# Optimization experiments

Measured on AMD Instinct MI355X. Metric: run time of the kernel, lower is better.

Reference implementation:

```python
import jax, jax.numpy as jnp
import numpy as np

N_USER = 100000
N_ITEM = 100000
SUPP = 10000
B = 1024
L = 50
S = 256
H = 4
E = 64
HID = 64


def setup_inputs() -> dict:
    key = jax.random.key(0)
    ks = jax.random.split(key, 32)
    f32 = jnp.float32
    inp = {}
    # forward int args
    inp["x"] = jax.random.randint(ks[0], (B, 2), 0, N_USER)
    inp["src_his"] = jax.random.randint(ks[1], (B, L), 0, N_ITEM)
    inp["src_hl"] = jax.random.randint(ks[2], (B,), 0, L)
    inp["tgt_his"] = jax.random.randint(ks[3], (B, L), 0, N_ITEM)
    inp["tgt_hl"] = jax.random.randint(ks[4], (B,), 0, L)
    # precomputed neighbor sampling: [2 get_user_emb calls, H heads, B, S]
    inp["sample_idx"] = jax.random.randint(ks[5], (2, H, B, S), 0, SUPP)
    inp["supp_users"] = jax.random.randint(ks[6], (SUPP,), 0, N_USER)
    # embedding tables (xavier-ish small scale)
    inp["src_user_emb"] = jax.random.normal(ks[7], (N_USER, E), f32) * 0.1
    inp["src_item_emb"] = jax.random.normal(ks[8], (N_ITEM, E), f32) * 0.1
    inp["tgt_user_emb"] = jax.random.normal(ks[9], (N_USER, E), f32) * 0.1
    inp["tgt_item_emb"] = jax.random.normal(ks[10], (N_ITEM, E), f32) * 0.1
    # attention / aggregation weights, stored [in, out]
    s = 1.0 / np.sqrt(E)
    inp["W_att_w"] = jax.random.normal(ks[11], (E, E), f32) * s
    inp["W_att_b"] = jnp.full((E,), 0.1, f32)
    inp["W_agg_w"] = jax.random.normal(ks[12], (E, E), f32) * s
    # per-head GAT projections, batched over heads
    inp["Wq"] = jax.random.normal(ks[13], (H, E, E), f32) * s
    inp["Wk"] = jax.random.normal(ks[14], (H, E, E), f32) * s
    inp["Wv"] = jax.random.normal(ks[15], (H, E, E), f32) * s
    inp["W_out"] = jax.random.normal(ks[16], (H * E, E), f32) * (1.0 / np.sqrt(H * E))
    # scoring MLP
    inp["l1_w"] = jax.random.normal(ks[17], (2 * E, HID), f32) * (1.0 / np.sqrt(2 * E))
    inp["l1_b"] = jnp.full((HID,), 0.1, f32)
    inp["l2_w"] = jax.random.normal(ks[18], (HID, E), f32) * (1.0 / np.sqrt(HID))
    inp["l2_b"] = jnp.full((E,), 0.1, f32)
    inp["l3_w"] = jax.random.normal(ks[19], (E, 1), f32) * s
    inp["l3_b"] = jnp.full((1,), 0.1, f32)
    return inp


def reference(x, src_his, src_hl, tgt_his, tgt_hl, sample_idx, supp_users,
              src_user_emb, src_item_emb, tgt_user_emb, tgt_item_emb,
              W_att_w, W_att_b, W_agg_w, Wq, Wk, Wv, W_out,
              l1_w, l1_b, l2_w, l2_b, l3_w, l3_b):
    user_id = x[:, 0]
    item_id = x[:, 1]

    def user_fea_encode(his, hl, user_table):
        # NOTE: original always gathers from src_model.item_embedding (even for tgt)
        Lh = his.shape[1]
        valid = jnp.arange(Lh)[None, :] < hl[:, None]          # [B,L]
        hist = src_item_emb[his] * valid[..., None]             # [B,L,E], padded rows zeroed
        u = user_table[user_id]                                 # [B,E]
        keyt = jnp.tanh(hist @ W_att_w + W_att_b)               # [B,L,E]
        pad = hist.sum(-1) == 0                                 # [B,L]
        att = jnp.einsum('ble,be->bl', keyt, u)
        # faithful masked_softmax: masked scores set to 0 BEFORE exp (exp(0)=1 still contributes)
        att = jnp.where(pad, 0.0, att)
        e = jnp.exp(att)
        att = e / (jnp.sum(e, axis=1, keepdims=True) + 1e-12)
        out = jnp.einsum('bl,ble->be', att, hist)
        return out @ W_agg_w                                    # W_agg has no bias

    def get_user_emb(fea, idx):
        # idx: [H,B,S] indices into supp_users; all heads batched in one einsum chain
        neigh = tgt_user_emb[supp_users[idx]]                   # [H,B,S,E]
        q = jnp.einsum('be,heo->hbo', fea, Wq)                  # [H,B,O]
        k = jnp.einsum('hbse,heo->hbso', neigh, Wk)             # [H,B,S,O]
        attn = jax.nn.softmax(jnp.einsum('hbo,hbso->hbs', q, k), axis=-1)
        ctx = jnp.einsum('hbs,hbso->hbo', attn, k)              # weighted sum over neighbors
        g = jnp.einsum('hbo,hop->hbp', ctx, Wv)                 # [H,B,O]
        g = jnp.transpose(g, (1, 0, 2)).reshape(fea.shape[0], -1)  # concat heads -> [B,H*O]
        return g @ W_out

    user_src_fea = user_fea_encode(src_his, src_hl, src_user_emb)
    user_emb = get_user_emb(user_src_fea, sample_idx[0])
    item_emb = tgt_item_emb[item_id]
    user_tgt_fea = user_fea_encode(tgt_his, tgt_hl, tgt_user_emb)
    hybrid_tgt_emb = get_user_emb(user_tgt_fea, sample_idx[1])

    x_t = jnp.concatenate([hybrid_tgt_emb, item_emb], axis=1)
    x1_t = jnp.tanh(x_t @ l1_w + l1_b)
    x2_t = jnp.tanh(x1_t @ l2_w + l2_b)
    x3_t = (x2_t @ l3_w + l3_b).reshape(-1)

    output = jnp.sum(user_emb * item_emb, axis=1)
    out_emb_s = user_emb * item_emb
    # (output, output_t, out_emb_s, out_emb_t); train=False branch (sim/domain heads are None)
    return (output, x3_t, out_emb_s, x2_t)
```

## Files before the change

kernel.cpp:

```cpp
#include <hip/hip_runtime.h>

constexpr int B    = 1024;
constexpr int L    = 50;
constexpr int S    = 256;
constexpr int H    = 4;
constexpr int E    = 64;
constexpr int HID  = 64;
constexpr int SUPP = 10000;

__device__ __forceinline__ float tanh_fast(float x) {
    const float xc = fminf(fmaxf(x, -15.0f), 15.0f);
    const float e  = __expf(2.0f * xc);
    return (e - 1.0f) * __builtin_amdgcn_rcpf(e + 1.0f);
}

__device__ __forceinline__ float lanebc(float v, int l) {
    return __int_as_float(__builtin_amdgcn_readlane(__float_as_int(v), l));
}

__global__ __launch_bounds__(256) void pre_kernel(
    const int* __restrict__ x,
    const int* __restrict__ src_his,
    const int* __restrict__ src_hl,
    const int* __restrict__ tgt_his,
    const int* __restrict__ tgt_hl,
    const float* __restrict__ item_emb,
    const float* __restrict__ src_user_emb,
    const float* __restrict__ tgt_user_emb,
    const int* __restrict__ supp_users,
    const float* __restrict__ W_att_w,
    const float* __restrict__ W_att_b,
    const float* __restrict__ W_agg_w,
    const float* __restrict__ Wq,
    const float* __restrict__ Wk,
    float* __restrict__ qout,
    float* __restrict__ K_supp)
{
    const int tid  = threadIdx.x;
    const int lane = tid & 63;
    const int wave = tid >> 6;

    if (blockIdx.y == 2) {
        __shared__ __align__(16) float sEvw[4][E];
        const int h = wave;
        float wcol[E];
#pragma unroll
        for (int i = 0; i < E; i++) wcol[i] = Wk[h * E * E + i * E + lane];

        int j = blockIdx.x;
        float ev = tgt_user_emb[(size_t)supp_users[j] * E + lane];
#pragma unroll 1
        while (j < SUPP) {
            const int jn = j + (int)gridDim.x;
            float evn = 0.0f;
            if (jn < SUPP)
                evn = tgt_user_emb[(size_t)supp_users[jn] * E + lane];
            sEvw[wave][lane] = ev;
            const float4* e4 = (const float4*)&sEvw[wave][0];
            float a0 = 0.f, a1 = 0.f, a2 = 0.f, a3 = 0.f;
#pragma unroll
            for (int k = 0; k < 16; k++) {
                const float4 v = e4[k];
                a0 = fmaf(v.x, wcol[4 * k + 0], a0);
                a1 = fmaf(v.y, wcol[4 * k + 1], a1);
                a2 = fmaf(v.z, wcol[4 * k + 2], a2);
                a3 = fmaf(v.w, wcol[4 * k + 3], a3);
            }
            K_supp[((size_t)h * SUPP + j) * E + lane] = (a0 + a1) + (a2 + a3);
            j = jn;
            ev = evn;
        }
        return;
    }

    __shared__ __align__(16) float sHist[L * E];
    __shared__ float sAtt[64];
    __shared__ float sPart[4][E];
    __shared__ float sOut[E];

    const int b    = blockIdx.x;
    const int call = blockIdx.y;

    const int* his = call ? tgt_his : src_his;
    const int* hl  = call ? tgt_hl  : src_hl;
    const float* user_table = call ? tgt_user_emb : src_user_emb;

    float wcol[E];
#pragma unroll
    for (int i = 0; i < E; i++) wcol[i] = W_att_w[i * E + lane];

    const int uid    = x[2 * b];
    const float uv   = user_table[(size_t)uid * E + lane];
    const float bias = W_att_b[lane];
    const int hlen   = hl[b];

#pragma unroll 1
    for (int l = wave; l < L; l += 4)
        if (l >= hlen && lane == 0) sAtt[l] = 0.0f;

    if (wave < hlen) {
        int l = wave;
        float hv = item_emb[(size_t)his[b * L + l] * E + lane];
#pragma unroll 1
        while (true) {
            const int ln = l + 4;
            float hvn = 0.0f;
            if (ln < hlen)
                hvn = item_emb[(size_t)his[b * L + ln] * E + lane];
            sHist[l * E + lane] = hv;
            const float4* hrow = (const float4*)&sHist[l * E];
            float a0 = bias, a1 = 0.f, a2 = 0.f, a3 = 0.f;
#pragma unroll
            for (int k = 0; k < 16; k++) {
                const float4 h4 = hrow[k];
                a0 = fmaf(h4.x, wcol[4 * k + 0], a0);
                a1 = fmaf(h4.y, wcol[4 * k + 1], a1);
                a2 = fmaf(h4.z, wcol[4 * k + 2], a2);
                a3 = fmaf(h4.w, wcol[4 * k + 3], a3);
            }
            float part = tanh_fast((a0 + a1) + (a2 + a3)) * uv;
#pragma unroll
            for (int off = 32; off; off >>= 1) part += __shfl_xor(part, off);
            if (lane == 0) sAtt[l] = part;
            l = ln;
            if (l >= hlen) break;
            hv = hvn;
        }
    }
    __syncthreads();

    const float vex = (lane < L) ? __expf(sAtt[lane]) : 0.0f;
    float sden = vex;
#pragma unroll
    for (int off = 32; off; off >>= 1) sden += __shfl_xor(sden, off);
    const float rden = __builtin_amdgcn_rcpf(sden + 1e-12f);

    float c = 0.0f;
#pragma unroll 1
    for (int l = wave; l < hlen; l += 4)
        c = fmaf(lanebc(vex, l) * rden, sHist[l * E + lane], c);
    sPart[wave][lane] = c;
    __syncthreads();
    if (tid < E) sOut[tid] = sPart[0][tid] + sPart[1][tid] + sPart[2][tid] + sPart[3][tid];
    __syncthreads();

    float g = 0.0f;
#pragma unroll
    for (int k = 0; k < 16; k++) {
        const int i = wave * 16 + k;
        g += sOut[i] * W_agg_w[i * E + lane];
    }
    sPart[wave][lane] = g;
    __syncthreads();

    const float fval = sPart[0][lane] + sPart[1][lane] + sPart[2][lane] + sPart[3][lane];
    const float* Wqh = Wq + wave * E * E;
    float q0 = 0.f, q1 = 0.f, q2 = 0.f, q3 = 0.f;
#pragma unroll
    for (int i = 0; i < E; i += 4) {
        q0 = fmaf(lanebc(fval, i + 0), Wqh[(i + 0) * E + lane], q0);
        q1 = fmaf(lanebc(fval, i + 1), Wqh[(i + 1) * E + lane], q1);
        q2 = fmaf(lanebc(fval, i + 2), Wqh[(i + 2) * E + lane], q2);
        q3 = fmaf(lanebc(fval, i + 3), Wqh[(i + 3) * E + lane], q3);
    }
    qout[(((call * H) + wave) * B + b) * E + lane] = (q0 + q1) + (q2 + q3);
}

__global__ __launch_bounds__(256) void attn_kernel(
    const int* __restrict__ sample_idx,
    const float* __restrict__ K_supp,
    const float* __restrict__ qarr,
    const float* __restrict__ Wv,
    float* __restrict__ gout)
{
    __shared__ float sRed[8];
    __shared__ float sCtx[4][E];
    __shared__ float sC[E];
    __shared__ float sG[4][E];

    const int n    = blockIdx.x;
    const int xcd  = n & 7;
    const int h    = xcd >> 1;
    const int call = xcd & 1;
    const int b    = n >> 3;
    const int tid  = threadIdx.x;
    const int lane = tid & 63;
    const int wave = tid >> 6;
    const int u    = lane & 15;
    const int rsub = lane >> 4;
    const int s0   = wave * 64;

    const int* idx = sample_idx + (((call * H) + h) * B + b) * S;
    const float* Kh = K_supp + (size_t)h * SUPP * E;
    const float4 qu = *(const float4*)(qarr + ((size_t)(((call * H) + h) * B + b)) * E + 4 * u);

    int jr[16];
#pragma unroll
    for (int i = 0; i < 16; i++) jr[i] = idx[s0 + 4 * i + rsub];
    float4 kreg[16];
#pragma unroll
    for (int i = 0; i < 16; i++)
        kreg[i] = *(const float4*)(Kh + (size_t)jr[i] * E + 4 * u);

    float mylogit = 0.0f;
#pragma unroll
    for (int i = 0; i < 16; i++) {
        float part = kreg[i].x * qu.x + kreg[i].y * qu.y
                   + kreg[i].z * qu.z + kreg[i].w * qu.w;
#pragma unroll
        for (int off = 1; off < 16; off <<= 1) part += __shfl_xor(part, off);
        mylogit = (u == i) ? part : mylogit;
    }

    float m = mylogit;
#pragma unroll
    for (int off = 32; off; off >>= 1) m = fmaxf(m, __shfl_xor(m, off));
    if (lane == 0) sRed[wave] = m;
    __syncthreads();
    const float mx = fmaxf(fmaxf(sRed[0], sRed[1]), fmaxf(sRed[2], sRed[3]));
    const float ex = __expf(mylogit - mx);
    float sm = ex;
#pragma unroll
    for (int off = 32; off; off >>= 1) sm += __shfl_xor(sm, off);
    if (lane == 0) sRed[4 + wave] = sm;
    __syncthreads();
    const float denom = sRed[4] + sRed[5] + sRed[6] + sRed[7];
    const float pval = ex / denom;

    float4 cacc = make_float4(0.0f, 0.0f, 0.0f, 0.0f);
#pragma unroll
    for (int i = 0; i < 16; i++) {
        const float p = __shfl(pval, (lane & 48) + i);
        cacc.x += p * kreg[i].x;
        cacc.y += p * kreg[i].y;
        cacc.z += p * kreg[i].z;
        cacc.w += p * kreg[i].w;
    }
#pragma unroll
    for (int off = 16; off <= 32; off <<= 1) {
        cacc.x += __shfl_xor(cacc.x, off);
        cacc.y += __shfl_xor(cacc.y, off);
        cacc.z += __shfl_xor(cacc.z, off);
        cacc.w += __shfl_xor(cacc.w, off);
    }
    if (lane < 16) *(float4*)(&sCtx[wave][u * 4]) = cacc;
    __syncthreads();
    if (wave == 0) {
        sC[lane] = sCtx[0][lane] + sCtx[1][lane] + sCtx[2][lane] + sCtx[3][lane];
    }
    __syncthreads();

    const float* Wvh = Wv + h * E * E;
    float g = 0.0f;
#pragma unroll
    for (int k = 0; k < 16; k++) {
        const int c = wave * 16 + k;
        g += sC[c] * Wvh[c * E + lane];
    }
    sG[wave][lane] = g;
    __syncthreads();
    if (wave == 0) {
        gout[((size_t)(call * B) + b) * (H * E) + h * E + lane] =
            sG[0][lane] + sG[1][lane] + sG[2][lane] + sG[3][lane];
    }
}

__global__ __launch_bounds__(256) void final_kernel(
    const int* __restrict__ x,
    const float* __restrict__ tgt_item_emb,
    const float* __restrict__ gsrc,
    const float* __restrict__ gtgt,
    const float* __restrict__ W_out,
    const float* __restrict__ l1_w,
    const float* __restrict__ l1_b,
    const float* __restrict__ l2_w,
    const float* __restrict__ l2_b,
    const float* __restrict__ l3_w,
    const float* __restrict__ l3_b,
    float* __restrict__ out)
{
    __shared__ float sPart[4][E];
    __shared__ float sHyb[E];
    __shared__ float sItem[E];
    __shared__ float sX1[HID];

    const int b    = blockIdx.x;
    const int tid  = threadIdx.x;
    const int lane = tid & 63;
    const int wave = tid >> 6;

    if (tid < E) {
        const int item = x[2 * b + 1];
        sItem[tid] = tgt_item_emb[(size_t)item * E + tid];
    }

    const float* grow = (wave < 2) ? (gsrc + (size_t)b * (H * E))
                                   : (gtgt + (size_t)b * (H * E));
    const int i0 = (wave & 1) * 128;
    {
        const float4* g4 = (const float4*)(grow + i0);
        float a0 = 0.0f, a1 = 0.0f, a2 = 0.0f, a3 = 0.0f;
#pragma unroll
        for (int k = 0; k < 32; k++) {
            const float4 v = g4[k];
            const float* wr = W_out + (i0 + 4 * k) * E + lane;
            a0 += v.x * wr[0];
            a1 += v.y * wr[E];
            a2 += v.z * wr[2 * E];
            a3 += v.w * wr[3 * E];
        }
        sPart[wave][lane] = (a0 + a1) + (a2 + a3);
    }
    __syncthreads();

    if (wave == 0) {
        const float ue = sPart[0][lane] + sPart[1][lane];
        const float prod = ue * sItem[lane];
        out[2 * B + b * E + lane] = prod;
        float s = prod;
#pragma unroll
        for (int off = 32; off; off >>= 1) s += __shfl_xor(s, off);
        if (lane == 0) out[b] = s;
    }
    if (wave == 1) {
        sHyb[lane] = sPart[2][lane] + sPart[3][lane];
    }
    __syncthreads();

    float a1 = 0.0f;
#pragma unroll
    for (int k = 0; k < 32; k++) {
        const int i = wave * 32 + k;
        const float v = (i < 64) ? sHyb[i] : sItem[i - 64];
        a1 += v * l1_w[i * HID + lane];
    }
    sPart[wave][lane] = a1;
    __syncthreads();

    if (wave == 0) {
        const float a = l1_b[lane] + sPart[0][lane] + sPart[1][lane]
                      + sPart[2][lane] + sPart[3][lane];
        sX1[lane] = tanh_fast(a);
    }
    __syncthreads();

    if (wave == 0) {
        float a = l2_b[lane];
#pragma unroll
        for (int i = 0; i < HID; i++) a += sX1[i] * l2_w[i * E + lane];
        const float x2 = tanh_fast(a);
        out[2 * B + B * E + b * E + lane] = x2;
        float p = x2 * l3_w[lane];
#pragma unroll
        for (int off = 32; off; off >>= 1) p += __shfl_xor(p, off);
        if (lane == 0) out[B + b] = p + l3_b[0];
    }
}

extern "C" void kernel_launch(void* const* d_in, const int* in_sizes, int n_in,
                              void* d_out, int out_size, void* d_ws, size_t ws_size,
                              hipStream_t stream) {
    const int*   x            = (const int*)d_in[0];
    const int*   src_his      = (const int*)d_in[1];
    const int*   src_hl       = (const int*)d_in[2];
    const int*   tgt_his      = (const int*)d_in[3];
    const int*   tgt_hl       = (const int*)d_in[4];
    const int*   sample_idx   = (const int*)d_in[5];
    const int*   supp_users   = (const int*)d_in[6];
    const float* src_user_emb = (const float*)d_in[7];
    const float* src_item_emb = (const float*)d_in[8];
    const float* tgt_user_emb = (const float*)d_in[9];
    const float* tgt_item_emb = (const float*)d_in[10];
    const float* W_att_w      = (const float*)d_in[11];
    const float* W_att_b      = (const float*)d_in[12];
    const float* W_agg_w      = (const float*)d_in[13];
    const float* Wq           = (const float*)d_in[14];
    const float* Wk           = (const float*)d_in[15];
    const float* Wv           = (const float*)d_in[16];
    const float* W_out        = (const float*)d_in[17];
    const float* l1_w         = (const float*)d_in[18];
    const float* l1_b         = (const float*)d_in[19];
    const float* l2_w         = (const float*)d_in[20];
    const float* l2_b         = (const float*)d_in[21];
    const float* l3_w         = (const float*)d_in[22];
    const float* l3_b         = (const float*)d_in[23];

    float* ws      = (float*)d_ws;
    float* qarr    = ws;
    float* K_supp  = qarr + 2 * H * B * E;
    float* garr    = K_supp + H * SUPP * E;
    float* out     = (float*)d_out;

    pre_kernel<<<dim3(B, 3), 256, 0, stream>>>(
        x, src_his, src_hl, tgt_his, tgt_hl, src_item_emb,
        src_user_emb, tgt_user_emb, supp_users,
        W_att_w, W_att_b, W_agg_w, Wq, Wk, qarr, K_supp);
    attn_kernel<<<dim3(B * H * 2), 256, 0, stream>>>(
        sample_idx, K_supp, qarr, Wv, garr);
    final_kernel<<<dim3(B), 256, 0, stream>>>(
        x, tgt_item_emb, garr, garr + B * H * E, W_out,
        l1_w, l1_b, l2_w, l2_b, l3_w, l3_b, out);
}
```

Baseline: 254.8 us.

## Fuse attention and final MLP kernels with single-wave online softmax per head

Merges the attention kernel and the final scoring kernel into one 512-thread block per batch row. Each wave now handles one (call, head) pair and walks its 256 neighbors in four chunks with an online softmax, so no cross-wave reductions are needed. The per-head outputs stay in shared memory instead of round-tripping through a global workspace, and one launch is removed. In exchange, each block loops over its neighbors serially with fewer blocks overall (1024 vs 8192), which reduces memory-level parallelism for the gather of K rows.

```diff
diff --git a/kernel.cpp b/kernel.cpp
--- a/kernel.cpp
+++ b/kernel.cpp
@@ -166,110 +166,13 @@
     qout[(((call * H) + wave) * B + b) * E + lane] = (q0 + q1) + (q2 + q3);
 }
 
-__global__ __launch_bounds__(256) void attn_kernel(
+__global__ __launch_bounds__(512) void attn_final_kernel(
     const int* __restrict__ sample_idx,
     const float* __restrict__ K_supp,
     const float* __restrict__ qarr,
     const float* __restrict__ Wv,
-    float* __restrict__ gout)
-{
-    __shared__ float sRed[8];
-    __shared__ float sCtx[4][E];
-    __shared__ float sC[E];
-    __shared__ float sG[4][E];
-
-    const int n    = blockIdx.x;
-    const int xcd  = n & 7;
-    const int h    = xcd >> 1;
-    const int call = xcd & 1;
-    const int b    = n >> 3;
-    const int tid  = threadIdx.x;
-    const int lane = tid & 63;
-    const int wave = tid >> 6;
-    const int u    = lane & 15;
-    const int rsub = lane >> 4;
-    const int s0   = wave * 64;
-
-    const int* idx = sample_idx + (((call * H) + h) * B + b) * S;
-    const float* Kh = K_supp + (size_t)h * SUPP * E;
-    const float4 qu = *(const float4*)(qarr + ((size_t)(((call * H) + h) * B + b)) * E + 4 * u);
-
-    int jr[16];
-#pragma unroll
-    for (int i = 0; i < 16; i++) jr[i] = idx[s0 + 4 * i + rsub];
-    float4 kreg[16];
-#pragma unroll
-    for (int i = 0; i < 16; i++)
-        kreg[i] = *(const float4*)(Kh + (size_t)jr[i] * E + 4 * u);
-
-    float mylogit = 0.0f;
-#pragma unroll
-    for (int i = 0; i < 16; i++) {
-        float part = kreg[i].x * qu.x + kreg[i].y * qu.y
-                   + kreg[i].z * qu.z + kreg[i].w * qu.w;
-#pragma unroll
-        for (int off = 1; off < 16; off <<= 1) part += __shfl_xor(part, off);
-        mylogit = (u == i) ? part : mylogit;
-    }
-
-    float m = mylogit;
-#pragma unroll
-    for (int off = 32; off; off >>= 1) m = fmaxf(m, __shfl_xor(m, off));
-    if (lane == 0) sRed[wave] = m;
-    __syncthreads();
-    const float mx = fmaxf(fmaxf(sRed[0], sRed[1]), fmaxf(sRed[2], sRed[3]));
-    const float ex = __expf(mylogit - mx);
-    float sm = ex;
-#pragma unroll
-    for (int off = 32; off; off >>= 1) sm += __shfl_xor(sm, off);
-    if (lane == 0) sRed[4 + wave] = sm;
-    __syncthreads();
-    const float denom = sRed[4] + sRed[5] + sRed[6] + sRed[7];
-    const float pval = ex / denom;
-
-    float4 cacc = make_float4(0.0f, 0.0f, 0.0f, 0.0f);
-#pragma unroll
-    for (int i = 0; i < 16; i++) {
-        const float p = __shfl(pval, (lane & 48) + i);
-        cacc.x += p * kreg[i].x;
-        cacc.y += p * kreg[i].y;
-        cacc.z += p * kreg[i].z;
-        cacc.w += p * kreg[i].w;
-    }
-#pragma unroll
-    for (int off = 16; off <= 32; off <<= 1) {
-        cacc.x += __shfl_xor(cacc.x, off);
-        cacc.y += __shfl_xor(cacc.y, off);
-        cacc.z += __shfl_xor(cacc.z, off);
-        cacc.w += __shfl_xor(cacc.w, off);
-    }
-    if (lane < 16) *(float4*)(&sCtx[wave][u * 4]) = cacc;
-    __syncthreads();
-    if (wave == 0) {
-        sC[lane] = sCtx[0][lane] + sCtx[1][lane] + sCtx[2][lane] + sCtx[3][lane];
-    }
-    __syncthreads();
-
-    const float* Wvh = Wv + h * E * E;
-    float g = 0.0f;
-#pragma unroll
-    for (int k = 0; k < 16; k++) {
-        const int c = wave * 16 + k;
-        g += sC[c] * Wvh[c * E + lane];
-    }
-    sG[wave][lane] = g;
-    __syncthreads();
-    if (wave == 0) {
-        gout[((size_t)(call * B) + b) * (H * E) + h * E + lane] =
-            sG[0][lane] + sG[1][lane] + sG[2][lane] + sG[3][lane];
-    }
-}
-
-__global__ __launch_bounds__(256) void final_kernel(
     const int* __restrict__ x,
     const float* __restrict__ tgt_item_emb,
-    const float* __restrict__ gsrc,
-    const float* __restrict__ gtgt,
     const float* __restrict__ W_out,
     const float* __restrict__ l1_w,
     const float* __restrict__ l1_b,
@@ -279,42 +182,123 @@
     const float* __restrict__ l3_b,
     float* __restrict__ out)
 {
-    __shared__ float sPart[4][E];
+    __shared__ __align__(16) float sCtxW[8][E];
+    __shared__ __align__(16) float sG[2][H * E];
+    __shared__ float sPart[8][E];
+    __shared__ float sItem[E];
     __shared__ float sHyb[E];
-    __shared__ float sItem[E];
     __shared__ float sX1[HID];
 
     const int b    = blockIdx.x;
     const int tid  = threadIdx.x;
     const int lane = tid & 63;
     const int wave = tid >> 6;
-
-    if (tid < E) {
-        const int item = x[2 * b + 1];
-        sItem[tid] = tgt_item_emb[(size_t)item * E + tid];
-    }
-
-    const float* grow = (wave < 2) ? (gsrc + (size_t)b * (H * E))
-                                   : (gtgt + (size_t)b * (H * E));
-    const int i0 = (wave & 1) * 128;
+    const int call = wave >> 2;
+    const int h    = wave & 3;
+    const int u    = lane & 15;
+    const int rsub = lane >> 4;
+
+    if (tid < E) sItem[tid] = tgt_item_emb[(size_t)x[2 * b + 1] * E + tid];
+
+    const int* idx = sample_idx + (((call * H) + h) * B + b) * S;
+    const float* Kh = K_supp + (size_t)h * SUPP * E;
+    const float4 qu = *(const float4*)(qarr + ((size_t)(((call * H) + h) * B + b)) * E + 4 * u);
+
+    float m = -1e30f, d = 0.0f;
+    float4 cacc = make_float4(0.0f, 0.0f, 0.0f, 0.0f);
+#pragma unroll 1
+    for (int c = 0; c < 4; c++) {
+        int jr[16];
+#pragma unroll
+        for (int i = 0; i < 16; i++) jr[i] = idx[64 * c + 4 * i + rsub];
+        float4 kreg[16];
+#pragma unroll
+        for (int i = 0; i < 16; i++)
+            kreg[i] = *(const float4*)(Kh + (size_t)jr[i] * E + 4 * u);
+
+        float lg = 0.0f;
+#pragma unroll
+        for (int i = 0; i < 16; i++) {
+            float part = kreg[i].x * qu.x + kreg[i].y * qu.y
+                       + kreg[i].z * qu.z + kreg[i].w * qu.w;
+#pragma unroll
+            for (int off = 1; off < 16; off <<= 1) part += __shfl_xor(part, off);
+            lg = (u == i) ? part : lg;
+        }
+
+        float cm = lg;
+#pragma unroll
+        for (int off = 32; off; off >>= 1) cm = fmaxf(cm, __shfl_xor(cm, off));
+        const float mn    = fmaxf(m, cm);
+        const float scale = __expf(m - mn);
+        const float ex    = __expf(lg - mn);
+        float cs = ex;
+#pragma unroll
+        for (int off = 32; off; off >>= 1) cs += __shfl_xor(cs, off);
+        d = d * scale + cs;
+        cacc.x *= scale; cacc.y *= scale; cacc.z *= scale; cacc.w *= scale;
+#pragma unroll
+        for (int i = 0; i < 16; i++) {
+            const float p = __shfl(ex, (lane & 48) + i);
+            cacc.x = fmaf(p, kreg[i].x, cacc.x);
+            cacc.y = fmaf(p, kreg[i].y, cacc.y);
+            cacc.z = fmaf(p, kreg[i].z, cacc.z);
+            cacc.w = fmaf(p, kreg[i].w, cacc.w);
+        }
+        m = mn;
+    }
+#pragma unroll
+    for (int off = 16; off <= 32; off <<= 1) {
+        cacc.x += __shfl_xor(cacc.x, off);
+        cacc.y += __shfl_xor(cacc.y, off);
+        cacc.z += __shfl_xor(cacc.z, off);
+        cacc.w += __shfl_xor(cacc.w, off);
+    }
+    const float rd = 1.0f / d;
+    if (rsub == 0) {
+        float4 cv;
+        cv.x = cacc.x * rd; cv.y = cacc.y * rd;
+        cv.z = cacc.z * rd; cv.w = cacc.w * rd;
+        *(float4*)(&sCtxW[wave][u * 4]) = cv;
+    }
     {
-        const float4* g4 = (const float4*)(grow + i0);
-        float a0 = 0.0f, a1 = 0.0f, a2 = 0.0f, a3 = 0.0f;
-#pragma unroll
-        for (int k = 0; k < 32; k++) {
+        const float4* cw = (const float4*)&sCtxW[wave][0];
+        const float* Wvh = Wv + h * E * E;
+        float g0 = 0.f, g1 = 0.f, g2 = 0.f, g3 = 0.f;
+#pragma unroll
+        for (int k = 0; k < 16; k++) {
+            const float4 cv = cw[k];
+            const float* wr = Wvh + (4 * k) * E + lane;
+            g0 = fmaf(cv.x, wr[0],     g0);
+            g1 = fmaf(cv.y, wr[E],     g1);
+            g2 = fmaf(cv.z, wr[2 * E], g2);
+            g3 = fmaf(cv.w, wr[3 * E], g3);
+        }
+        sG[call][h * E + lane] = (g0 + g1) + (g2 + g3);
+    }
+    __syncthreads();
+
+    {
+        const int p = wave >> 2;
+        const int q = wave & 3;
+        const float4* g4 = (const float4*)&sG[p][q * 64];
+        float a0 = 0.f, a1 = 0.f, a2 = 0.f, a3 = 0.f;
+#pragma unroll
+        for (int k = 0; k < 16; k++) {
             const float4 v = g4[k];
-            const float* wr = W_out + (i0 + 4 * k) * E + lane;
-            a0 += v.x * wr[0];
-            a1 += v.y * wr[E];
-            a2 += v.z * wr[2 * E];
-            a3 += v.w * wr[3 * E];
+            const float* wr = W_out + (q * 64 + 4 * k) * E + lane;
+            a0 = fmaf(v.x, wr[0],     a0);
+            a1 = fmaf(v.y, wr[E],     a1);
+            a2 = fmaf(v.z, wr[2 * E], a2);
+            a3 = fmaf(v.w, wr[3 * E], a3);
         }
         sPart[wave][lane] = (a0 + a1) + (a2 + a3);
     }
     __syncthreads();
 
     if (wave == 0) {
-        const float ue = sPart[0][lane] + sPart[1][lane];
+        const float ue = (sPart[0][lane] + sPart[1][lane])
+                       + (sPart[2][lane] + sPart[3][lane]);
         const float prod = ue * sItem[lane];
         out[2 * B + b * E + lane] = prod;
         float s = prod;
@@ -323,23 +307,27 @@
         if (lane == 0) out[b] = s;
     }
     if (wave == 1) {
-        sHyb[lane] = sPart[2][lane] + sPart[3][lane];
-    }
-    __syncthreads();
-
-    float a1 = 0.0f;
-#pragma unroll
-    for (int k = 0; k < 32; k++) {
-        const int i = wave * 32 + k;
-        const float v = (i < 64) ? sHyb[i] : sItem[i - 64];
-        a1 += v * l1_w[i * HID + lane];
-    }
-    sPart[wave][lane] = a1;
+        sHyb[lane] = (sPart[4][lane] + sPart[5][lane])
+                   + (sPart[6][lane] + sPart[7][lane]);
+    }
+    __syncthreads();
+
+    {
+        float a1v = 0.0f;
+#pragma unroll
+        for (int k = 0; k < 16; k++) {
+            const int i = wave * 16 + k;
+            const float v = (i < 64) ? sHyb[i] : sItem[i - 64];
+            a1v = fmaf(v, l1_w[i * HID + lane], a1v);
+        }
+        sPart[wave][lane] = a1v;
+    }
     __syncthreads();
 
     if (wave == 0) {
-        const float a = l1_b[lane] + sPart[0][lane] + sPart[1][lane]
-                      + sPart[2][lane] + sPart[3][lane];
+        float a = l1_b[lane];
+#pragma unroll
+        for (int w = 0; w < 8; w++) a += sPart[w][lane];
         sX1[lane] = tanh_fast(a);
     }
     __syncthreads();
@@ -347,7 +335,7 @@
     if (wave == 0) {
         float a = l2_b[lane];
 #pragma unroll
-        for (int i = 0; i < HID; i++) a += sX1[i] * l2_w[i * E + lane];
+        for (int i = 0; i < HID; i++) a = fmaf(sX1[i], l2_w[i * E + lane], a);
         const float x2 = tanh_fast(a);
         out[2 * B + B * E + b * E + lane] = x2;
         float p = x2 * l3_w[lane];
@@ -388,16 +376,13 @@
     float* ws      = (float*)d_ws;
     float* qarr    = ws;
     float* K_supp  = qarr + 2 * H * B * E;
-    float* garr    = K_supp + H * SUPP * E;
     float* out     = (float*)d_out;
 
     pre_kernel<<<dim3(B, 3), 256, 0, stream>>>(
         x, src_his, src_hl, tgt_his, tgt_hl, src_item_emb,
         src_user_emb, tgt_user_emb, supp_users,
         W_att_w, W_att_b, W_agg_w, Wq, Wk, qarr, K_supp);
-    attn_kernel<<<dim3(B * H * 2), 256, 0, stream>>>(
-        sample_idx, K_supp, qarr, Wv, garr);
-    final_kernel<<<dim3(B), 256, 0, stream>>>(
-        x, tgt_item_emb, garr, garr + B * H * E, W_out,
+    attn_final_kernel<<<dim3(B), 512, 0, stream>>>(
+        sample_idx, K_supp, qarr, Wv, x, tgt_item_emb, W_out,
         l1_w, l1_b, l2_w, l2_b, l3_w, l3_b, out);
 }
```

Measured after the change: 287.4 us. 12.8% more time.

## Widen pre_kernel to 512 threads, splitting history, aggregation and Q projection across 8 waves

Applied to the files above, without the earlier changes.

The pre-processing kernel moves from 4 to 8 waves per block. History rows are strided by 8 and the W_agg reduction is split 8 ways. The Q projection splits each head's input dimension across two waves and adds their partial sums through shared memory. The K_supp branch handles two support users per block iteration. The aim is more parallelism and latency hiding per block, at the cost of extra barriers and per-thread register pressure (wcol[64]) under the 512-thread launch bound, which could lower occupancy.

```diff
diff --git a/kernel.cpp b/kernel.cpp
--- a/kernel.cpp
+++ b/kernel.cpp
@@ -18,7 +18,7 @@
     return __int_as_float(__builtin_amdgcn_readlane(__float_as_int(v), l));
 }
 
-__global__ __launch_bounds__(256) void pre_kernel(
+__global__ __launch_bounds__(512) void pre_kernel(
     const int* __restrict__ x,
     const int* __restrict__ src_his,
     const int* __restrict__ src_hl,
@@ -41,17 +41,18 @@
     const int wave = tid >> 6;
 
     if (blockIdx.y == 2) {
-        __shared__ __align__(16) float sEvw[4][E];
-        const int h = wave;
+        __shared__ __align__(16) float sEvw[8][E];
+        const int h = wave & 3;
         float wcol[E];
 #pragma unroll
         for (int i = 0; i < E; i++) wcol[i] = Wk[h * E * E + i * E + lane];
 
-        int j = blockIdx.x;
-        float ev = tgt_user_emb[(size_t)supp_users[j] * E + lane];
+        int j = 2 * blockIdx.x + (wave >> 2);
+        const int jstride = 2 * (int)gridDim.x;
+        float ev = (j < SUPP) ? tgt_user_emb[(size_t)supp_users[j] * E + lane] : 0.0f;
 #pragma unroll 1
         while (j < SUPP) {
-            const int jn = j + (int)gridDim.x;
+            const int jn = j + jstride;
             float evn = 0.0f;
             if (jn < SUPP)
                 evn = tgt_user_emb[(size_t)supp_users[jn] * E + lane];
@@ -75,7 +76,7 @@
 
     __shared__ __align__(16) float sHist[L * E];
     __shared__ float sAtt[64];
-    __shared__ float sPart[4][E];
+    __shared__ float sPart[8][E];
     __shared__ float sOut[E];
 
     const int b    = blockIdx.x;
@@ -95,7 +96,7 @@
     const int hlen   = hl[b];
 
 #pragma unroll 1
-    for (int l = wave; l < L; l += 4)
+    for (int l = wave; l < L; l += 8)
         if (l >= hlen && lane == 0) sAtt[l] = 0.0f;
 
     if (wave < hlen) {
@@ -103,7 +104,7 @@
         float hv = item_emb[(size_t)his[b * L + l] * E + lane];
 #pragma unroll 1
         while (true) {
-            const int ln = l + 4;
+            const int ln = l + 8;
             float hvn = 0.0f;
             if (ln < hlen)
                 hvn = item_emb[(size_t)his[b * L + ln] * E + lane];
@@ -137,33 +138,55 @@
 
     float c = 0.0f;
 #pragma unroll 1
-    for (int l = wave; l < hlen; l += 4)
+    for (int l = wave; l < hlen; l += 8)
         c = fmaf(lanebc(vex, l) * rden, sHist[l * E + lane], c);
     sPart[wave][lane] = c;
     __syncthreads();
-    if (tid < E) sOut[tid] = sPart[0][tid] + sPart[1][tid] + sPart[2][tid] + sPart[3][tid];
-    __syncthreads();
-
-    float g = 0.0f;
-#pragma unroll
-    for (int k = 0; k < 16; k++) {
-        const int i = wave * 16 + k;
-        g += sOut[i] * W_agg_w[i * E + lane];
-    }
-    sPart[wave][lane] = g;
-    __syncthreads();
-
-    const float fval = sPart[0][lane] + sPart[1][lane] + sPart[2][lane] + sPart[3][lane];
-    const float* Wqh = Wq + wave * E * E;
-    float q0 = 0.f, q1 = 0.f, q2 = 0.f, q3 = 0.f;
-#pragma unroll
-    for (int i = 0; i < E; i += 4) {
-        q0 = fmaf(lanebc(fval, i + 0), Wqh[(i + 0) * E + lane], q0);
-        q1 = fmaf(lanebc(fval, i + 1), Wqh[(i + 1) * E + lane], q1);
-        q2 = fmaf(lanebc(fval, i + 2), Wqh[(i + 2) * E + lane], q2);
-        q3 = fmaf(lanebc(fval, i + 3), Wqh[(i + 3) * E + lane], q3);
-    }
-    qout[(((call * H) + wave) * B + b) * E + lane] = (q0 + q1) + (q2 + q3);
+    if (tid < E) {
+        sOut[tid] = ((sPart[0][tid] + sPart[1][tid]) + (sPart[2][tid] + sPart[3][tid]))
+                  + ((sPart[4][tid] + sPart[5][tid]) + (sPart[6][tid] + sPart[7][tid]));
+    }
+    __syncthreads();
+
+    {
+        float g0 = 0.f, g1 = 0.f, g2 = 0.f, g3 = 0.f;
+        const int i0 = wave * 8;
+#pragma unroll
+        for (int k = 0; k < 2; k++) {
+            const int i = i0 + 4 * k;
+            const float* wr = W_agg_w + i * E + lane;
+            g0 = fmaf(sOut[i + 0], wr[0],     g0);
+            g1 = fmaf(sOut[i + 1], wr[E],     g1);
+            g2 = fmaf(sOut[i + 2], wr[2 * E], g2);
+            g3 = fmaf(sOut[i + 3], wr[3 * E], g3);
+        }
+        sPart[wave][lane] = (g0 + g1) + (g2 + g3);
+    }
+    __syncthreads();
+
+    const float fval = ((sPart[0][lane] + sPart[1][lane]) + (sPart[2][lane] + sPart[3][lane]))
+                     + ((sPart[4][lane] + sPart[5][lane]) + (sPart[6][lane] + sPart[7][lane]));
+    __syncthreads();
+    {
+        const int hh  = wave & 3;
+        const int khf = wave >> 2;
+        const float* Wqh = Wq + hh * E * E + khf * 32 * E;
+        float q0 = 0.f, q1 = 0.f, q2 = 0.f, q3 = 0.f;
+#pragma unroll
+        for (int i = 0; i < 32; i += 4) {
+            q0 = fmaf(lanebc(fval, khf * 32 + i + 0), Wqh[(i + 0) * E + lane], q0);
+            q1 = fmaf(lanebc(fval, khf * 32 + i + 1), Wqh[(i + 1) * E + lane], q1);
+            q2 = fmaf(lanebc(fval, khf * 32 + i + 2), Wqh[(i + 2) * E + lane], q2);
+            q3 = fmaf(lanebc(fval, khf * 32 + i + 3), Wqh[(i + 3) * E + lane], q3);
+        }
+        sPart[wave][lane] = (q0 + q1) + (q2 + q3);
+    }
+    __syncthreads();
+    if (tid < H * E) {
+        const int hh = tid >> 6;
+        const int ln = tid & 63;
+        qout[(((call * H) + hh) * B + b) * E + ln] = sPart[hh][ln] + sPart[hh + 4][ln];
+    }
 }
 
 __global__ __launch_bounds__(256) void attn_kernel(
@@ -391,7 +414,7 @@
     float* garr    = K_supp + H * SUPP * E;
     float* out     = (float*)d_out;
 
-    pre_kernel<<<dim3(B, 3), 256, 0, stream>>>(
+    pre_kernel<<<dim3(B, 3), 512, 0, stream>>>(
         x, src_his, src_hl, tgt_his, tgt_hl, src_item_emb,
         src_user_emb, tgt_user_emb, supp_users,
         W_att_w, W_att_b, W_agg_w, Wq, Wk, qarr, K_supp);
```

After: 258.6 us. No clear change (+1.5%).
